# Kernel optimization log

Hardware: AMD Instinct MI355X
Metric: run time of the kernel (lower is better)

Reference implementation:

```python
import jax, jax.numpy as jnp
import numpy as np

N_NODES = 50000
N_EDGES = 1600000
F_IN = 128
E_DIM = 16
F_HID = 16
K_CHEB = 4
MAX_ELEM = 8
MLP_HID = 4
F_OUT = 8


def setup_inputs() -> dict:
    key = jax.random.key(0)
    ks = jax.random.split(key, 20)
    s = 0.1
    inp = {
        "x": jax.random.normal(ks[0], (N_NODES, F_IN), jnp.float32),
        "edge_index": jax.random.randint(ks[1], (2, N_EDGES), 0, N_NODES),
        "edge_attr": jax.random.normal(ks[2], (N_EDGES, E_DIM), jnp.float32),
        # GATv2Conv params (heads=1)
        "Wl": jax.random.normal(ks[3], (F_IN, F_HID), jnp.float32) * s,
        "bl": jnp.zeros((F_HID,), jnp.float32),
        "Wr": jax.random.normal(ks[4], (F_IN, F_HID), jnp.float32) * s,
        "br": jnp.zeros((F_HID,), jnp.float32),
        "We": jax.random.normal(ks[5], (E_DIM, F_HID), jnp.float32) * s,
        "att": jax.random.normal(ks[6], (F_HID,), jnp.float32) * s,
        "gat_bias": jnp.zeros((F_HID,), jnp.float32),
        # GConvGRU: 6 ChebConvs in order [x_z, h_z, x_r, h_r, x_h, h_h]
        "cheb_W": jax.random.normal(ks[7], (6, K_CHEB, F_HID, F_HID), jnp.float32) * s,
        "cheb_b": jnp.zeros((6, F_HID), jnp.float32),
        # MLPAggregation MLP: 8*16 -> 4 -> 8 (batch-norm at init stats == identity)
        "W1": jax.random.normal(ks[8], (MAX_ELEM * F_HID, MLP_HID), jnp.float32) * s,
        "b1": jnp.zeros((MLP_HID,), jnp.float32),
        "W2": jax.random.normal(ks[9], (MLP_HID, F_OUT), jnp.float32) * s,
        "b2": jnp.zeros((F_OUT,), jnp.float32),
    }
    return inp


def _gatv2(x, src, dst, edge_attr, Wl, bl, Wr, br, We, att, gat_bias):
    N = x.shape[0]
    # add_self_loops with fill_value='mean' on edge_attr (mean of incoming attrs per dst)
    cnt = jax.ops.segment_sum(jnp.ones_like(src, dtype=x.dtype), dst, num_segments=N)
    ea_mean = jax.ops.segment_sum(edge_attr, dst, num_segments=N) / jnp.maximum(cnt, 1.0)[:, None]
    loop = jnp.arange(N)
    src2 = jnp.concatenate([src, loop])
    dst2 = jnp.concatenate([dst, loop])
    ea2 = jnp.concatenate([edge_attr, ea_mean], axis=0)
    xl = x @ Wl + bl          # source transform [N, F_HID]
    xr = x @ Wr + br          # target transform
    em = ea2 @ We             # edge transform   [E+N, F_HID]
    m = xl[src2] + xr[dst2] + em
    alpha = jax.nn.leaky_relu(m, 0.2) @ att  # [E+N]
    amax = jax.ops.segment_max(alpha, dst2, num_segments=N)
    ex = jnp.exp(alpha - amax[dst2])
    denom = jax.ops.segment_sum(ex, dst2, num_segments=N)
    w = ex / (denom[dst2] + 1e-16)
    out = jax.ops.segment_sum(w[:, None] * xl[src2], dst2, num_segments=N)
    return out + gat_bias


def _cheb(x, src, dst, norm, W, b):
    # ChebConv with sym normalization, lambda_max=2 -> scaled Laplacian = -D^-1/2 A D^-1/2
    N = x.shape[0]
    def matvec(v):
        return jax.ops.segment_sum(norm[:, None] * v[src], dst, num_segments=N)
    Tx0 = x
    out = Tx0 @ W[0]
    Tx1 = matvec(Tx0)
    out = out + Tx1 @ W[1]
    for k in range(2, W.shape[0]):
        Tx2 = 2.0 * matvec(Tx1) - Tx0
        out = out + Tx2 @ W[k]
        Tx0, Tx1 = Tx1, Tx2
    return out + b


def reference(x, edge_index, edge_attr, Wl, bl, Wr, br, We, att, gat_bias,
              cheb_W, cheb_b, W1, b1, W2, b2):
    N = x.shape[0]
    src, dst = edge_index[0], edge_index[1]
    # --- GATv2Conv snapshot ---
    h = _gatv2(x, src, dst, edge_attr, Wl, bl, Wr, br, We, att, gat_bias)  # [N,16]
    # --- Chebyshev Laplacian normalization (remove self loops, sym norm) ---
    w = (src != dst).astype(x.dtype)
    deg = jax.ops.segment_sum(w, src, num_segments=N)
    dinv = jnp.where(deg > 0, jax.lax.rsqrt(jnp.maximum(deg, 1e-12)), 0.0)
    norm = -dinv[src] * w * dinv[dst]
    # --- GConvGRU (single step, H0 = 0) ---
    H = jnp.zeros_like(h)
    Z = jax.nn.sigmoid(_cheb(h, src, dst, norm, cheb_W[0], cheb_b[0])
                       + _cheb(H, src, dst, norm, cheb_W[1], cheb_b[1]))
    R = jax.nn.sigmoid(_cheb(h, src, dst, norm, cheb_W[2], cheb_b[2])
                       + _cheb(H, src, dst, norm, cheb_W[3], cheb_b[3]))
    Ht = jnp.tanh(_cheb(h, src, dst, norm, cheb_W[4], cheb_b[4])
                  + _cheb(R * H, src, dst, norm, cheb_W[5], cheb_b[5]))
    H = Z * H + (1.0 - Z) * Ht  # [N,16]
    # --- MLPAggregation with idx = arange(N)+1: each node its own segment ---
    # dense batch [N+1, MAX_ELEM, 16]: segment k>0 holds H[k-1] in slot 0, rest zeros.
    flat = jnp.concatenate([H, jnp.zeros((N, (MAX_ELEM - 1) * F_HID), H.dtype)], axis=1)
    dense = jnp.concatenate([jnp.zeros((1, MAX_ELEM * F_HID), H.dtype), flat], axis=0)
    out = jax.nn.relu(dense @ W1 + b1) @ W2 + b2  # [N+1, 8]
    return out
```

## Files before the change

kernel.cpp:

```cpp
#include <hip/hip_runtime.h>
#include <cmath>


constexpr int N = 50000;
constexpr int E = 1600000;

__global__ __launch_bounds__(256)
void k_node_transform(const float* __restrict__ x,
                      const float* __restrict__ Wl, const float* __restrict__ bl,
                      const float* __restrict__ Wr, const float* __restrict__ br,
                      float* __restrict__ xl, float* __restrict__ xr) {
    __shared__ float sWl[128 * 16];
    __shared__ float sWr[128 * 16];
    int t = threadIdx.x;
    for (int i = t; i < 2048; i += 256) { sWl[i] = Wl[i]; sWr[i] = Wr[i]; }
    __syncthreads();
    int f = t & 15, nl = t >> 4;
    int n = blockIdx.x * 16 + nl;
    const float4* xv = reinterpret_cast<const float4*>(x + (size_t)n * 128);
    float aL = bl[f], aR = br[f];
#pragma unroll 8
    for (int k4 = 0; k4 < 32; ++k4) {
        float4 v = xv[k4];
        int k = k4 * 4;
        aL += v.x * sWl[(k + 0) * 16 + f]; aR += v.x * sWr[(k + 0) * 16 + f];
        aL += v.y * sWl[(k + 1) * 16 + f]; aR += v.y * sWr[(k + 1) * 16 + f];
        aL += v.z * sWl[(k + 2) * 16 + f]; aR += v.z * sWr[(k + 2) * 16 + f];
        aL += v.w * sWl[(k + 3) * 16 + f]; aR += v.w * sWr[(k + 3) * 16 + f];
    }
    xl[n * 16 + f] = aL;
    xr[n * 16 + f] = aR;
}

__global__ __launch_bounds__(256)
void k_hist(const int* __restrict__ ei, int* __restrict__ cnt_in, int* __restrict__ deg_out) {
    int e = blockIdx.x * 256 + threadIdx.x;
    int s = ei[e], d = ei[E + e];
    atomicAdd(&cnt_in[d], 1);
    if (s != d) atomicAdd(&deg_out[s], 1);
}

__global__ __launch_bounds__(1024)
void k_scan(const int* __restrict__ cnt, int* __restrict__ rowptr, int n) {
    __shared__ int ssum[1024];
    int t = threadIdx.x;
    const int chunk = 52;
    int lo = t * chunk;
    int hi = lo + chunk; if (hi > n) hi = n; if (lo > n) lo = n;
    int s = 0;
    for (int i = lo; i + 3 < hi; i += 4) {
        int4 v = *reinterpret_cast<const int4*>(cnt + i);
        s += v.x + v.y + v.z + v.w;
    }
    ssum[t] = s;
    __syncthreads();
    for (int off = 1; off < 1024; off <<= 1) {
        int v = (t >= off) ? ssum[t - off] : 0;
        __syncthreads();
        ssum[t] += v;
        __syncthreads();
    }
    int prefix = (t == 0) ? 0 : ssum[t - 1];
    for (int i = lo; i < hi; ++i) { rowptr[i] = prefix; prefix += cnt[i]; }
    if (t == 0) rowptr[n] = ssum[1023];
}

__global__ __launch_bounds__(256)
void k_edge_place(const int* __restrict__ ei, const int* __restrict__ rowptr,
                  int* __restrict__ ctr, int2* __restrict__ sedge) {
    int e = blockIdx.x * 256 + threadIdx.x;
    int s = ei[e], d = ei[E + e];
    int p = rowptr[d] + atomicAdd(&ctr[d], 1);
    sedge[p] = make_int2(s, e);
}

__global__ __launch_bounds__(256)
void k_gat(const int* __restrict__ rowptr, const int2* __restrict__ sedge,
           const float* __restrict__ ea, const float* __restrict__ xl,
           const float* __restrict__ xr, const int* __restrict__ deg_out,
           const float* __restrict__ We, const float* __restrict__ att,
           const float* __restrict__ gat_bias,
           const float* __restrict__ Wz0, const float* __restrict__ Wh0,
           float* __restrict__ h, float* __restrict__ hs,
           float* __restrict__ accz, float* __restrict__ acch,
           float* __restrict__ dinv) {
    __shared__ float sWe[256], sWz[256], sWh[256];
    __shared__ float satt[16];
    __shared__ float strans[16][16][17];
    __shared__ float sbuf[16][17];
    int t = threadIdx.x;
    sWe[t] = We[t]; sWz[t] = Wz0[t]; sWh[t] = Wh0[t];
    if (t < 16) satt[t] = att[t];
    __syncthreads();
    int f = t & 15, nl = t >> 4;
    int n = blockIdx.x * 16 + nl;
    int lo = rowptr[n], hi = rowptr[n + 1];
    float xrn[16];
    {
        const float4* xr4 = reinterpret_cast<const float4*>(xr + (size_t)n * 16);
#pragma unroll
        for (int j = 0; j < 4; ++j) {
            float4 v = xr4[j];
            xrn[4*j] = v.x; xrn[4*j+1] = v.y; xrn[4*j+2] = v.z; xrn[4*j+3] = v.w;
        }
    }
    float m_l = -3.0e38f, den_l = 0.f;
    float num_l[16], emacc[16];
#pragma unroll
    for (int j = 0; j < 16; ++j) { num_l[j] = 0.f; emacc[j] = 0.f; }
    for (int i = lo + f; i < hi; i += 16) {
        int2 se = sedge[i];
        const float4* ea4 = reinterpret_cast<const float4*>(ea + (size_t)se.y * 16);
        const float4* xl4 = reinterpret_cast<const float4*>(xl + (size_t)se.x * 16);
        float a[16], xs[16];
#pragma unroll
        for (int j = 0; j < 4; ++j) {
            float4 v = ea4[j]; a[4*j] = v.x; a[4*j+1] = v.y; a[4*j+2] = v.z; a[4*j+3] = v.w;
            float4 u = xl4[j]; xs[4*j] = u.x; xs[4*j+1] = u.y; xs[4*j+2] = u.z; xs[4*j+3] = u.w;
        }
        float alpha = 0.f;
#pragma unroll
        for (int f2 = 0; f2 < 16; ++f2) {
            float em = 0.f;
#pragma unroll
            for (int j = 0; j < 16; ++j) em += a[j] * sWe[j * 16 + f2];
            emacc[f2] += em;
            float m = xs[f2] + xrn[f2] + em;
            m = m > 0.f ? m : 0.2f * m;
            alpha += m * satt[f2];
        }
        float ex;
        if (alpha > m_l) {
            float sc = expf(m_l - alpha);
            den_l *= sc;
#pragma unroll
            for (int j = 0; j < 16; ++j) num_l[j] *= sc;
            m_l = alpha; ex = 1.f;
        } else {
            ex = expf(alpha - m_l);
        }
        den_l += ex;
#pragma unroll
        for (int j = 0; j < 16; ++j) num_l[j] += ex * xs[j];
    }
    float M = m_l;
#pragma unroll
    for (int off = 1; off < 16; off <<= 1) M = fmaxf(M, __shfl_xor(M, off, 64));
    float s_l = expf(m_l - M);
    float den = den_l * s_l;
#pragma unroll
    for (int off = 1; off < 16; off <<= 1) den += __shfl_xor(den, off, 64);
#pragma unroll
    for (int j = 0; j < 16; ++j) strans[nl][f][j] = num_l[j] * s_l;
    __syncthreads();
    float num_f = 0.f;
#pragma unroll
    for (int j = 0; j < 16; ++j) num_f += strans[nl][j][f];
    __syncthreads();
#pragma unroll
    for (int j = 0; j < 16; ++j) strans[nl][f][j] = emacc[j];
    __syncthreads();
    float emsum_f = 0.f;
#pragma unroll
    for (int j = 0; j < 16; ++j) emsum_f += strans[nl][j][f];
    float cntf = (float)(hi - lo);
    float xlf = xl[n * 16 + f];
    float xrf = xr[n * 16 + f];
    float m0 = xlf + xrf + emsum_f / fmaxf(cntf, 1.f);
    m0 = m0 > 0.f ? m0 : 0.2f * m0;
    float c = m0 * satt[f];
#pragma unroll
    for (int off = 1; off < 16; off <<= 1) c += __shfl_xor(c, off, 64);
    float aloop = c;
    float Mf = fmaxf(M, aloop);
    float sc2 = expf(M - Mf);
    float exl = expf(aloop - Mf);
    num_f = num_f * sc2 + exl * xlf;
    float dent = den * sc2 + exl;
    float hv = num_f / (dent + 1e-16f) + gat_bias[f];
    float dg = (float)deg_out[n];
    float di = dg > 0.f ? rsqrtf(dg) : 0.f;
    h[n * 16 + f] = hv;
    hs[n * 16 + f] = di * hv;
    if (f == 0) dinv[n] = di;
    sbuf[nl][f] = hv;
    __syncthreads();
    float az = 0.f, ah = 0.f;
#pragma unroll
    for (int j = 0; j < 16; ++j) {
        float v = sbuf[nl][j];
        az += v * sWz[j * 16 + f];
        ah += v * sWh[j * 16 + f];
    }
    accz[n * 16 + f] = az;
    acch[n * 16 + f] = ah;
}

__global__ __launch_bounds__(256)
void k_mvcomb(const int* __restrict__ rowptr, const int2* __restrict__ sedge,
              const float* __restrict__ dinv, const float* __restrict__ Tins,
              const float* __restrict__ Tprev, float* __restrict__ Tstore,
              float* __restrict__ Tscale_store,
              const float* __restrict__ Wzk, const float* __restrict__ Whk,
              float* __restrict__ accz, float* __restrict__ acch, int mode) {
    __shared__ float sWz[256], sWh[256];
    __shared__ float st[16][17];
    int t = threadIdx.x;
    sWz[t] = Wzk[t]; sWh[t] = Whk[t];
    int f = t & 15, nl = t >> 4;
    int n = blockIdx.x * 16 + nl;
    int lo = rowptr[n], hi = rowptr[n + 1];
    float acc = 0.f;
    for (int i = lo; i < hi; ++i) {
        int s = sedge[i].x;
        if (s != n) acc += Tins[s * 16 + f];
    }
    float di = dinv[n];
    float tv = -di * acc;
    if (mode) tv = 2.f * tv - Tprev[n * 16 + f];
    if (Tstore)       Tstore[n * 16 + f] = tv;
    if (Tscale_store) Tscale_store[n * 16 + f] = di * tv;
    st[nl][f] = tv;
    __syncthreads();
    float az = accz[n * 16 + f], ah = acch[n * 16 + f];
#pragma unroll
    for (int j = 0; j < 16; ++j) {
        float v = st[nl][j];
        az += v * sWz[j * 16 + f];
        ah += v * sWh[j * 16 + f];
    }
    accz[n * 16 + f] = az;
    acch[n * 16 + f] = ah;
}

__global__ __launch_bounds__(256)
void k_mvfinal(const int* __restrict__ rowptr, const int2* __restrict__ sedge,
               const float* __restrict__ dinv, const float* __restrict__ Tins,
               const float* __restrict__ Tprev,
               const float* __restrict__ Wzk, const float* __restrict__ Whk,
               const float* __restrict__ accz, const float* __restrict__ acch,
               const float* __restrict__ cheb_b,
               const float* __restrict__ W1, const float* __restrict__ b1,
               const float* __restrict__ W2, const float* __restrict__ b2,
               float* __restrict__ out) {
    __shared__ float sWz[256], sWh[256];
    __shared__ float st[16][17];
    int t = threadIdx.x;
    sWz[t] = Wzk[t]; sWh[t] = Whk[t];
    int f = t & 15, nl = t >> 4;
    int n = blockIdx.x * 16 + nl;
    int lo = rowptr[n], hi = rowptr[n + 1];
    float acc = 0.f;
    for (int i = lo; i < hi; ++i) {
        int s = sedge[i].x;
        if (s != n) acc += Tins[s * 16 + f];
    }
    float tv = -dinv[n] * acc;
    tv = 2.f * tv - Tprev[n * 16 + f];
    st[nl][f] = tv;
    __syncthreads();
    float az = accz[n * 16 + f], ah = acch[n * 16 + f];
#pragma unroll
    for (int j = 0; j < 16; ++j) {
        float v = st[nl][j];
        az += v * sWz[j * 16 + f];
        ah += v * sWh[j * 16 + f];
    }
    float z  = 1.f / (1.f + expf(-(az + cheb_b[f] + cheb_b[16 + f])));
    float ht = tanhf(ah + cheb_b[64 + f] + cheb_b[80 + f]);
    float H = (1.f - z) * ht;
    __syncthreads();
    st[nl][f] = H;
    __syncthreads();
    float hid[4];
#pragma unroll
    for (int cc = 0; cc < 4; ++cc) {
        float v = b1[cc];
#pragma unroll
        for (int j = 0; j < 16; ++j) v += st[nl][j] * W1[j * 4 + cc];
        hid[cc] = fmaxf(v, 0.f);
    }
    if (f < 8) {
        float v = b2[f];
#pragma unroll
        for (int cc = 0; cc < 4; ++cc) v += hid[cc] * W2[cc * 8 + f];
        out[(size_t)(n + 1) * 8 + f] = v;
    }
    if (blockIdx.x == 0 && t == 0) {
        float h0[4];
#pragma unroll
        for (int cc = 0; cc < 4; ++cc) h0[cc] = fmaxf(b1[cc], 0.f);
#pragma unroll
        for (int o = 0; o < 8; ++o) {
            float v = b2[o];
#pragma unroll
            for (int cc = 0; cc < 4; ++cc) v += h0[cc] * W2[cc * 8 + o];
            out[o] = v;
        }
    }
}

extern "C" void kernel_launch(void* const* d_in, const int* in_sizes, int n_in,
                              void* d_out, int out_size, void* d_ws, size_t ws_size,
                              hipStream_t stream) {
    const float* x    = (const float*)d_in[0];
    const int*   ei   = (const int*)d_in[1];
    const float* ea   = (const float*)d_in[2];
    const float* Wl   = (const float*)d_in[3];
    const float* bl   = (const float*)d_in[4];
    const float* Wr   = (const float*)d_in[5];
    const float* br   = (const float*)d_in[6];
    const float* We   = (const float*)d_in[7];
    const float* att  = (const float*)d_in[8];
    const float* gatb = (const float*)d_in[9];
    const float* chW  = (const float*)d_in[10];
    const float* chb  = (const float*)d_in[11];
    const float* W1   = (const float*)d_in[12];
    const float* b1   = (const float*)d_in[13];
    const float* W2   = (const float*)d_in[14];
    const float* b2   = (const float*)d_in[15];
    float* out = (float*)d_out;

    char* w = (char*)d_ws;
    size_t off = 0;
    auto alloc = [&](size_t elems) {
        off = (off + 15) & ~(size_t)15;
        void* p = w + off;
        off += elems * 4;
        return p;
    };
    int*   cnt_in  = (int*)alloc(N);
    int*   deg_out = (int*)alloc(N);
    int*   ctr     = (int*)alloc(N);
    int*   rowptr  = (int*)alloc(N + 2);
    float* xl      = (float*)alloc(16 * N);
    float* xr      = (float*)alloc(16 * N);
    int2*  sedge   = (int2*)alloc(2 * (size_t)E);
    float* dinv    = (float*)alloc(N);
    float* h       = (float*)alloc(16 * N);
    float* hs      = (float*)alloc(16 * N);
    float* accz    = (float*)alloc(16 * N);
    float* acch    = (float*)alloc(16 * N);
    float* T1      = (float*)alloc(16 * N);
    float* Tsa     = (float*)alloc(16 * N);
    float* Tsb     = (float*)alloc(16 * N);
    (void)ws_size; (void)in_sizes; (void)n_in; (void)out_size;

    hipMemsetAsync(cnt_in, 0, (size_t)3 * N * sizeof(int), stream);

    k_node_transform<<<N / 16, 256, 0, stream>>>(x, Wl, bl, Wr, br, xl, xr);
    k_hist<<<E / 256, 256, 0, stream>>>(ei, cnt_in, deg_out);
    k_scan<<<1, 1024, 0, stream>>>(cnt_in, rowptr, N);
    k_edge_place<<<E / 256, 256, 0, stream>>>(ei, rowptr, ctr, sedge);
    k_gat<<<N / 16, 256, 0, stream>>>(rowptr, sedge, ea, xl, xr, deg_out, We, att,
                                      gatb, chW + 0 * 256, chW + 16 * 256,
                                      h, hs, accz, acch, dinv);
    k_mvcomb<<<N / 16, 256, 0, stream>>>(rowptr, sedge, dinv, hs, (const float*)nullptr,
                                         T1, Tsa, chW + 1 * 256, chW + 17 * 256,
                                         accz, acch, 0);
    k_mvcomb<<<N / 16, 256, 0, stream>>>(rowptr, sedge, dinv, Tsa, h,
                                         (float*)nullptr, Tsb, chW + 2 * 256, chW + 18 * 256,
                                         accz, acch, 1);
    k_mvfinal<<<N / 16, 256, 0, stream>>>(rowptr, sedge, dinv, Tsb, T1,
                                          chW + 3 * 256, chW + 19 * 256,
                                          accz, acch, chb, W1, b1, W2, b2, out);
}
```

Baseline: 794.6 us.

## Fuse node transform with histogram, compact source indices, branchless online softmax in GAT

The node feature transform and the edge histogram now run as one launch, with blocks split by index range, which removes a kernel launch and lets the two overlap. The GAT kernel also writes a compact int array of sorted source indices, so the three Chebyshev propagation kernels read 4 bytes per edge instead of 8. Other changes in the GAT kernel: xr is staged in shared memory instead of per-thread registers, the online-softmax update is made branchless at the cost of two exps per edge, and launch bounds request 3 blocks per SM to limit register use. The extra store in GAT and the added exp work trade against lower register pressure and less traffic in the later kernels.

```diff
diff --git a/kernel.cpp b/kernel.cpp
--- a/kernel.cpp
+++ b/kernel.cpp
@@ -4,12 +4,22 @@
 
 constexpr int N = 50000;
 constexpr int E = 1600000;
+constexpr int NT_BLOCKS = N / 16;
 
 __global__ __launch_bounds__(256)
-void k_node_transform(const float* __restrict__ x,
-                      const float* __restrict__ Wl, const float* __restrict__ bl,
-                      const float* __restrict__ Wr, const float* __restrict__ br,
-                      float* __restrict__ xl, float* __restrict__ xr) {
+void k_pre(const float* __restrict__ x,
+           const float* __restrict__ Wl, const float* __restrict__ bl,
+           const float* __restrict__ Wr, const float* __restrict__ br,
+           float* __restrict__ xl, float* __restrict__ xr,
+           const int* __restrict__ ei, int* __restrict__ cnt_in,
+           int* __restrict__ deg_out) {
+    if ((int)blockIdx.x >= NT_BLOCKS) {
+        int e = ((int)blockIdx.x - NT_BLOCKS) * 256 + threadIdx.x;
+        int s = ei[e], d = ei[E + e];
+        atomicAdd(&cnt_in[d], 1);
+        if (s != d) atomicAdd(&deg_out[s], 1);
+        return;
+    }
     __shared__ float sWl[128 * 16];
     __shared__ float sWr[128 * 16];
     int t = threadIdx.x;
@@ -32,14 +42,6 @@
     xr[n * 16 + f] = aR;
 }
 
-__global__ __launch_bounds__(256)
-void k_hist(const int* __restrict__ ei, int* __restrict__ cnt_in, int* __restrict__ deg_out) {
-    int e = blockIdx.x * 256 + threadIdx.x;
-    int s = ei[e], d = ei[E + e];
-    atomicAdd(&cnt_in[d], 1);
-    if (s != d) atomicAdd(&deg_out[s], 1);
-}
-
 __global__ __launch_bounds__(1024)
 void k_scan(const int* __restrict__ cnt, int* __restrict__ rowptr, int n) {
     __shared__ int ssum[1024];
@@ -74,42 +76,37 @@
     sedge[p] = make_int2(s, e);
 }
 
-__global__ __launch_bounds__(256)
+__global__ __launch_bounds__(256, 3)
 void k_gat(const int* __restrict__ rowptr, const int2* __restrict__ sedge,
            const float* __restrict__ ea, const float* __restrict__ xl,
            const float* __restrict__ xr, const int* __restrict__ deg_out,
            const float* __restrict__ We, const float* __restrict__ att,
            const float* __restrict__ gat_bias,
            const float* __restrict__ Wz0, const float* __restrict__ Wh0,
+           int* __restrict__ ssrc,
            float* __restrict__ h, float* __restrict__ hs,
            float* __restrict__ accz, float* __restrict__ acch,
            float* __restrict__ dinv) {
     __shared__ float sWe[256], sWz[256], sWh[256];
     __shared__ float satt[16];
+    __shared__ float sxr[16][17];
     __shared__ float strans[16][16][17];
     __shared__ float sbuf[16][17];
     int t = threadIdx.x;
     sWe[t] = We[t]; sWz[t] = Wz0[t]; sWh[t] = Wh0[t];
     if (t < 16) satt[t] = att[t];
-    __syncthreads();
     int f = t & 15, nl = t >> 4;
     int n = blockIdx.x * 16 + nl;
+    sxr[nl][f] = xr[n * 16 + f];
+    __syncthreads();
     int lo = rowptr[n], hi = rowptr[n + 1];
-    float xrn[16];
-    {
-        const float4* xr4 = reinterpret_cast<const float4*>(xr + (size_t)n * 16);
-#pragma unroll
-        for (int j = 0; j < 4; ++j) {
-            float4 v = xr4[j];
-            xrn[4*j] = v.x; xrn[4*j+1] = v.y; xrn[4*j+2] = v.z; xrn[4*j+3] = v.w;
-        }
-    }
     float m_l = -3.0e38f, den_l = 0.f;
     float num_l[16], emacc[16];
 #pragma unroll
     for (int j = 0; j < 16; ++j) { num_l[j] = 0.f; emacc[j] = 0.f; }
     for (int i = lo + f; i < hi; i += 16) {
         int2 se = sedge[i];
+        ssrc[i] = se.x;
         const float4* ea4 = reinterpret_cast<const float4*>(ea + (size_t)se.y * 16);
         const float4* xl4 = reinterpret_cast<const float4*>(xl + (size_t)se.x * 16);
         float a[16], xs[16];
@@ -121,27 +118,21 @@
         float alpha = 0.f;
 #pragma unroll
         for (int f2 = 0; f2 < 16; ++f2) {
-            float em = 0.f;
-#pragma unroll
-            for (int j = 0; j < 16; ++j) em += a[j] * sWe[j * 16 + f2];
-            emacc[f2] += em;
-            float m = xs[f2] + xrn[f2] + em;
+            float e2 = 0.f;
+#pragma unroll
+            for (int j = 0; j < 16; ++j) e2 += a[j] * sWe[j * 16 + f2];
+            emacc[f2] += e2;
+            float m = xs[f2] + sxr[nl][f2] + e2;
             m = m > 0.f ? m : 0.2f * m;
             alpha += m * satt[f2];
         }
-        float ex;
-        if (alpha > m_l) {
-            float sc = expf(m_l - alpha);
-            den_l *= sc;
-#pragma unroll
-            for (int j = 0; j < 16; ++j) num_l[j] *= sc;
-            m_l = alpha; ex = 1.f;
-        } else {
-            ex = expf(alpha - m_l);
-        }
-        den_l += ex;
-#pragma unroll
-        for (int j = 0; j < 16; ++j) num_l[j] += ex * xs[j];
+        float mnew = fmaxf(m_l, alpha);
+        float corr = expf(m_l - mnew);
+        float ex   = expf(alpha - mnew);
+        den_l = den_l * corr + ex;
+#pragma unroll
+        for (int j = 0; j < 16; ++j) num_l[j] = num_l[j] * corr + ex * xs[j];
+        m_l = mnew;
     }
     float M = m_l;
 #pragma unroll
@@ -165,7 +156,7 @@
     for (int j = 0; j < 16; ++j) emsum_f += strans[nl][j][f];
     float cntf = (float)(hi - lo);
     float xlf = xl[n * 16 + f];
-    float xrf = xr[n * 16 + f];
+    float xrf = sxr[nl][f];
     float m0 = xlf + xrf + emsum_f / fmaxf(cntf, 1.f);
     m0 = m0 > 0.f ? m0 : 0.2f * m0;
     float c = m0 * satt[f];
@@ -197,7 +188,7 @@
 }
 
 __global__ __launch_bounds__(256)
-void k_mvcomb(const int* __restrict__ rowptr, const int2* __restrict__ sedge,
+void k_mvcomb(const int* __restrict__ rowptr, const int* __restrict__ ssrc,
               const float* __restrict__ dinv, const float* __restrict__ Tins,
               const float* __restrict__ Tprev, float* __restrict__ Tstore,
               float* __restrict__ Tscale_store,
@@ -212,7 +203,7 @@
     int lo = rowptr[n], hi = rowptr[n + 1];
     float acc = 0.f;
     for (int i = lo; i < hi; ++i) {
-        int s = sedge[i].x;
+        int s = ssrc[i];
         if (s != n) acc += Tins[s * 16 + f];
     }
     float di = dinv[n];
@@ -234,7 +225,7 @@
 }
 
 __global__ __launch_bounds__(256)
-void k_mvfinal(const int* __restrict__ rowptr, const int2* __restrict__ sedge,
+void k_mvfinal(const int* __restrict__ rowptr, const int* __restrict__ ssrc,
                const float* __restrict__ dinv, const float* __restrict__ Tins,
                const float* __restrict__ Tprev,
                const float* __restrict__ Wzk, const float* __restrict__ Whk,
@@ -252,7 +243,7 @@
     int lo = rowptr[n], hi = rowptr[n + 1];
     float acc = 0.f;
     for (int i = lo; i < hi; ++i) {
-        int s = sedge[i].x;
+        int s = ssrc[i];
         if (s != n) acc += Tins[s * 16 + f];
     }
     float tv = -dinv[n] * acc;
@@ -336,6 +327,7 @@
     float* xl      = (float*)alloc(16 * N);
     float* xr      = (float*)alloc(16 * N);
     int2*  sedge   = (int2*)alloc(2 * (size_t)E);
+    int*   ssrc    = (int*)alloc(E);
     float* dinv    = (float*)alloc(N);
     float* h       = (float*)alloc(16 * N);
     float* hs      = (float*)alloc(16 * N);
@@ -348,20 +340,20 @@
 
     hipMemsetAsync(cnt_in, 0, (size_t)3 * N * sizeof(int), stream);
 
-    k_node_transform<<<N / 16, 256, 0, stream>>>(x, Wl, bl, Wr, br, xl, xr);
-    k_hist<<<E / 256, 256, 0, stream>>>(ei, cnt_in, deg_out);
+    k_pre<<<NT_BLOCKS + E / 256, 256, 0, stream>>>(x, Wl, bl, Wr, br, xl, xr,
+                                                   ei, cnt_in, deg_out);
     k_scan<<<1, 1024, 0, stream>>>(cnt_in, rowptr, N);
     k_edge_place<<<E / 256, 256, 0, stream>>>(ei, rowptr, ctr, sedge);
     k_gat<<<N / 16, 256, 0, stream>>>(rowptr, sedge, ea, xl, xr, deg_out, We, att,
                                       gatb, chW + 0 * 256, chW + 16 * 256,
-                                      h, hs, accz, acch, dinv);
-    k_mvcomb<<<N / 16, 256, 0, stream>>>(rowptr, sedge, dinv, hs, (const float*)nullptr,
+                                      ssrc, h, hs, accz, acch, dinv);
+    k_mvcomb<<<N / 16, 256, 0, stream>>>(rowptr, ssrc, dinv, hs, (const float*)nullptr,
                                          T1, Tsa, chW + 1 * 256, chW + 17 * 256,
                                          accz, acch, 0);
-    k_mvcomb<<<N / 16, 256, 0, stream>>>(rowptr, sedge, dinv, Tsa, h,
+    k_mvcomb<<<N / 16, 256, 0, stream>>>(rowptr, ssrc, dinv, Tsa, h,
                                          (float*)nullptr, Tsb, chW + 2 * 256, chW + 18 * 256,
                                          accz, acch, 1);
-    k_mvfinal<<<N / 16, 256, 0, stream>>>(rowptr, sedge, dinv, Tsb, T1,
+    k_mvfinal<<<N / 16, 256, 0, stream>>>(rowptr, ssrc, dinv, Tsb, T1,
                                           chW + 3 * 256, chW + 19 * 256,
                                           accz, acch, chb, W1, b1, W2, b2, out);
 }
```

Result: slower. 1.123 ms (+41.3%).
